# Kernel optimization log

Measured on AMD Instinct MI355X. Metric: run time of the kernel, lower is better.

## Reference

```python
import jax, jax.numpy as jnp
import numpy as np

B, T, H, D = 4, 2048, 16, 64
HID = H * D
ROPE_THETA = 10000.0


def _rope_tables(t, d, theta):
    # frequencies over half the head dim, duplicated to full head_dim
    inv_freq = 1.0 / (theta ** (np.arange(0, d, 2, dtype=np.float32) / d))  # (d/2,)
    pos = np.arange(t, dtype=np.float32)
    freqs = np.outer(pos, inv_freq)                      # (T, d/2)
    emb = np.concatenate([freqs, freqs], axis=-1)        # (T, d)
    return jnp.asarray(np.cos(emb)), jnp.asarray(np.sin(emb))


def setup_inputs() -> dict:
    key = jax.random.key(0)
    ks = jax.random.split(key, 5)
    s = 1.0 / np.sqrt(HID)
    cos, sin = _rope_tables(T, D, ROPE_THETA)
    return {
        "x": jax.random.normal(ks[0], (B, T, HID), dtype=jnp.float32),
        "cos": cos,
        "sin": sin,
        "wq": jax.random.normal(ks[1], (HID, HID), dtype=jnp.float32) * s,
        "wk": jax.random.normal(ks[2], (HID, HID), dtype=jnp.float32) * s,
        "wv": jax.random.normal(ks[3], (HID, HID), dtype=jnp.float32) * s,
        "wo": jax.random.normal(ks[4], (HID, HID), dtype=jnp.float32) * s,
    }


def _rotate_half(x):
    x1, x2 = jnp.split(x, 2, axis=-1)
    return jnp.concatenate([-x2, x1], axis=-1)


def reference(x, cos, sin, wq, wk, wv, wo):
    b, t, _ = x.shape
    # QKV projections (nn.Linear: y = x @ W^T), reshape to (B, H, T, D)
    q = (x @ wq.T).reshape(b, t, H, D).transpose(0, 2, 1, 3)
    k = (x @ wk.T).reshape(b, t, H, D).transpose(0, 2, 1, 3)
    v = (x @ wv.T).reshape(b, t, H, D).transpose(0, 2, 1, 3)
    # RoPE
    c = cos[None, None, :, :]
    s = sin[None, None, :, :]
    q = q * c + _rotate_half(q) * s
    k = k * c + _rotate_half(k) * s
    # causal SDPA
    scale = 1.0 / jnp.sqrt(jnp.asarray(D, dtype=x.dtype))
    scores = jnp.einsum("bhqd,bhkd->bhqk", q, k) * scale
    causal = jnp.tril(jnp.ones((t, t), dtype=bool))
    scores = jnp.where(causal[None, None], scores, jnp.finfo(scores.dtype).min)
    attn = jax.nn.softmax(scores, axis=-1)
    out = jnp.einsum("bhqk,bhkd->bhqd", attn, v)
    out = out.transpose(0, 2, 1, 3).reshape(b, t, HID)
    return out @ wo.T
```

## Files before the change

kernel.cpp:

```cpp
#include <hip/hip_runtime.h>

#define BSZ 4
#define TT 2048
#define NH 16
#define HD 64
#define HID 1024
#define BT 8192
#define BH 64

typedef unsigned short u16;
typedef unsigned int u32;
typedef unsigned long long u64;
typedef __attribute__((ext_vector_type(4))) float f32x4;
typedef __attribute__((ext_vector_type(8))) short bf16x8;

#define MFMA32(a, b, c) __builtin_amdgcn_mfma_f32_16x16x32_bf16(a, b, c, 0, 0, 0)

typedef const __attribute__((address_space(1))) u32* gp32;
typedef __attribute__((address_space(3))) u32* lp32;

__device__ __forceinline__ u16 f2bf(float f) {
    union { float f; u32 u; } x; x.f = f;
    u32 r = x.u + 0x7FFFu + ((x.u >> 16) & 1u);
    return (u16)(r >> 16);
}

__global__ __launch_bounds__(256) void cast_kernel(const float* __restrict__ src,
                                                   u16* __restrict__ dst, int n4) {
    int i = blockIdx.x * 256 + threadIdx.x;
    if (i >= n4) return;
    f32x4 v = *(const f32x4*)(src + (size_t)i * 4);
    uint2 u;
    u.x = (u32)f2bf(v[0]) | ((u32)f2bf(v[1]) << 16);
    u.y = (u32)f2bf(v[2]) | ((u32)f2bf(v[3]) << 16);
    *(uint2*)(dst + (size_t)i * 4) = u;
}

template<int MODE>
__global__ __launch_bounds__(256)
void gemm_bt(const u16* __restrict__ A, const u16* __restrict__ W,
             float* __restrict__ Cf, u16* __restrict__ qkv, u16* __restrict__ vt,
             const float* __restrict__ cosT, const float* __restrict__ sinT) {
    __shared__ u16 sh[128 * 128];
    u16* As = sh;
    u16* Bs = sh + 128 * 64;
    const int tid  = threadIdx.x;
    const int wv   = tid >> 6, lane = tid & 63;
    const int lrow = lane & 15, lk = lane >> 4;
    const int wm   = (wv & 1) * 64, wn = (wv >> 1) * 64;
    const int m0   = blockIdx.x * 128, n0 = blockIdx.y * 128;

    f32x4 acc[4][4] = {};

    for (int kk = 0; kk < HID; kk += 64) {
        __syncthreads();
        #pragma unroll
        for (int i = 0; i < 4; ++i) {
            int l16 = i * 256 + tid;
            int r = l16 >> 3, c = l16 & 7;
            int gc = (c ^ (r & 7)) * 8;
            __builtin_amdgcn_global_load_lds(
                (gp32)&A[(size_t)(m0 + r) * HID + kk + gc],
                (lp32)&As[l16 * 8], 16, 0, 0);
            __builtin_amdgcn_global_load_lds(
                (gp32)&W[(size_t)(n0 + r) * HID + kk + gc],
                (lp32)&Bs[l16 * 8], 16, 0, 0);
        }
        __syncthreads();

        #pragma unroll
        for (int k0 = 0; k0 < 64; k0 += 32) {
            bf16x8 af[4], bfr[4];
            #pragma unroll
            for (int i = 0; i < 4; ++i) {
                int row = wm + i * 16 + lrow;
                int pc  = ((k0 >> 3) + lk) ^ (row & 7);
                af[i] = *(const bf16x8*)&As[row * 64 + pc * 8];
            }
            #pragma unroll
            for (int j = 0; j < 4; ++j) {
                int row = wn + j * 16 + lrow;
                int pc  = ((k0 >> 3) + lk) ^ (row & 7);
                bfr[j] = *(const bf16x8*)&Bs[row * 64 + pc * 8];
            }
            #pragma unroll
            for (int i = 0; i < 4; ++i)
                #pragma unroll
                for (int j = 0; j < 4; ++j)
                    acc[i][j] = MFMA32(af[i], bfr[j], acc[i][j]);
        }
    }
    __syncthreads();

    if (MODE == 0) {
        if (blockIdx.y < 16) {
            const float QSC = (blockIdx.y < 8) ? 0.125f * 1.44269504f : 1.0f;
            #pragma unroll
            for (int i = 0; i < 4; ++i)
                #pragma unroll
                for (int r = 0; r < 4; ++r) {
                    int tl = (m0 + wm + i * 16 + lk * 4 + r) & (TT - 1);
                    #pragma unroll
                    for (int j = 0; j < 2; ++j) {
                        int dd = j * 16 + lrow;
                        float c = cosT[tl * HD + dd], s = sinT[tl * HD + dd];
                        float v1 = acc[i][j][r], v2 = acc[i][j + 2][r];
                        acc[i][j][r]     = (v1 * c - v2 * s) * QSC;
                        acc[i][j + 2][r] = (v2 * c + v1 * s) * QSC;
                    }
                }
        }
        #pragma unroll
        for (int i = 0; i < 4; ++i)
            #pragma unroll
            for (int j = 0; j < 4; ++j)
                #pragma unroll
                for (int r = 0; r < 4; ++r)
                    sh[(wm + i * 16 + lk * 4 + r) * 128 + wn + j * 16 + lrow] = f2bf(acc[i][j][r]);
        __syncthreads();
        const int b = m0 >> 11, tl0 = m0 & (TT - 1);
        if (blockIdx.y < 16) {
            #pragma unroll
            for (int p = 0; p < 8; ++p) {
                int idx = p * 256 + tid;
                int r = idx >> 4, c16 = idx & 15;
                f32x4 v = *(const f32x4*)&sh[r * 128 + c16 * 8];
                int nfull = n0 + c16 * 8;
                int proj = nfull >> 10, nl = nfull & 1023;
                int h = nl >> 6, d = nl & 63;
                u16* dst = qkv + (size_t)proj * BT * HID +
                           (((size_t)(b * NH + h) * TT + tl0 + r) * HD + d);
                *(f32x4*)dst = v;
            }
        } else {
            #pragma unroll
            for (int p = 0; p < 8; ++p) {
                int oc  = p * 256 + tid;
                int col = oc & 127;
                int t8  = oc >> 7;
                union { f32x4 v4; u16 u[8]; } u;
                #pragma unroll
                for (int j = 0; j < 8; ++j) u.u[j] = sh[(t8 * 8 + j) * 128 + col];
                int nl = ((n0 - 2048) + col);
                int h = nl >> 6, d = nl & 63;
                *(f32x4*)&vt[((size_t)(b * NH + h) * HD + d) * TT + tl0 + t8 * 8] = u.v4;
            }
        }
    } else {
        #pragma unroll
        for (int i = 0; i < 4; ++i)
            #pragma unroll
            for (int j = 0; j < 4; ++j)
                #pragma unroll
                for (int r = 0; r < 4; ++r) {
                    int m = m0 + wm + i * 16 + lk * 4 + r;
                    int n = n0 + wn + j * 16 + lrow;
                    Cf[(size_t)m * HID + n] = acc[i][j][r];
                }
    }
}

__device__ __forceinline__ u32 pkhu(float a, float b) {
    union { float f; u32 u; } xa, xb; xa.f = a; xb.f = b;
    return ((xa.u + 0x8000u) >> 16) | ((xb.u + 0x8000u) & 0xFFFF0000u);
}
__device__ __forceinline__ bf16x8 packP(const f32x4& a, const f32x4& b) {
    union { bf16x8 v; u32 w[4]; } u;
    u.w[0] = pkhu(a[0], a[1]); u.w[1] = pkhu(a[2], a[3]);
    u.w[2] = pkhu(b[0], b[1]); u.w[3] = pkhu(b[2], b[3]);
    return u.v;
}

__global__ __launch_bounds__(256)
void attn_kernel(const u16* __restrict__ q, const u16* __restrict__ k,
                 const u16* __restrict__ vt, u16* __restrict__ o) {
    __shared__ u16 Ks[64 * 72];
    __shared__ u16 Vts[64 * 72];
    const int tid  = threadIdx.x;
    const int w    = tid >> 6, lane = tid & 63;
    const int lrow = lane & 15, lk = lane >> 4;
    const int bh   = blockIdx.y;
    const int p    = blockIdx.x;
    const int q0a  = 64 * p, q0b = 64 * (31 - p);
    const size_t hb = (size_t)bh * TT * HD;

    bf16x8 qfa[2], qfb[2];
    #pragma unroll
    for (int kq = 0; kq < 2; ++kq) {
        qfa[kq] = *(const bf16x8*)&q[hb + (size_t)(q0a + w * 16 + lrow) * HD + kq * 32 + lk * 8];
        qfb[kq] = *(const bf16x8*)&q[hb + (size_t)(q0b + w * 16 + lrow) * HD + kq * 32 + lk * 8];
    }

    f32x4 oa[4] = {}, obc[4] = {};
    float lia = 0.f, lib = 0.f;

    const int r0 = tid >> 3, f0 = (tid & 7) * 8;
    const int r1 = (tid + 256) >> 3, f1 = (tid & 7) * 8;

    f32x4 pk0 = *(const f32x4*)&k[hb + (size_t)r0 * HD + f0];
    f32x4 pk1 = *(const f32x4*)&k[hb + (size_t)r1 * HD + f1];
    f32x4 pv0 = *(const f32x4*)&vt[hb + (size_t)r0 * TT + f0];
    f32x4 pv1 = *(const f32x4*)&vt[hb + (size_t)r1 * TT + f1];

    const int nIter = 32 - p;
    for (int it = 0; it < nIter; ++it) {
        const bool a_act = (it <= p);
        __syncthreads();
        *(f32x4*)&Ks[r0 * 72 + f0]  = pk0;
        *(f32x4*)&Ks[r1 * 72 + f1]  = pk1;
        *(f32x4*)&Vts[r0 * 72 + f0] = pv0;
        *(f32x4*)&Vts[r1 * 72 + f1] = pv1;
        __syncthreads();
        if (it + 1 < nIter) {
            const int nn = (it + 1) * 64;
            pk0 = *(const f32x4*)&k[hb + (size_t)(nn + r0) * HD + f0];
            pk1 = *(const f32x4*)&k[hb + (size_t)(nn + r1) * HD + f1];
            pv0 = *(const f32x4*)&vt[hb + (size_t)r0 * TT + nn + f0];
            pv1 = *(const f32x4*)&vt[hb + (size_t)r1 * TT + nn + f1];
        }

        bf16x8 kf0[4], kf1[4];
        #pragma unroll
        for (int mt = 0; mt < 4; ++mt) {
            kf0[mt] = *(const bf16x8*)&Ks[(mt * 16 + lrow) * 72 + lk * 8];
            kf1[mt] = *(const bf16x8*)&Ks[(mt * 16 + lrow) * 72 + 32 + lk * 8];
        }

        {
            f32x4 s[4] = {};
            #pragma unroll
            for (int mt = 0; mt < 4; ++mt) {
                s[mt] = MFMA32(kf0[mt], qfb[0], s[mt]);
                s[mt] = MFMA32(kf1[mt], qfb[1], s[mt]);
            }
            if (it == nIter - 1) {
                #pragma unroll
                for (int mt = 0; mt < 4; ++mt)
                    #pragma unroll
                    for (int r = 0; r < 4; ++r)
                        if (mt * 16 + lk * 4 + r > w * 16 + lrow) s[mt][r] = -1e30f;
            }
            #pragma unroll
            for (int mt = 0; mt < 4; ++mt)
                #pragma unroll
                for (int r = 0; r < 4; ++r) {
                    float pv = exp2f(s[mt][r]);
                    s[mt][r] = pv; lib += pv;
                }
            bf16x8 p0 = packP(s[0], s[1]), p1 = packP(s[2], s[3]);
            #pragma unroll
            for (int t2 = 0; t2 < 2; ++t2)
                #pragma unroll
                for (int dm = 0; dm < 4; ++dm) {
                    union { bf16x8 v; struct { u64 lo, hi; } u; } vf;
                    const u16* vrow = &Vts[(dm * 16 + lrow) * 72 + t2 * 32 + lk * 4];
                    vf.u.lo = *(const u64*)vrow;
                    vf.u.hi = *(const u64*)(vrow + 16);
                    obc[dm] = MFMA32(vf.v, t2 ? p1 : p0, obc[dm]);
                }
        }

        if (a_act) {
            f32x4 s[4] = {};
            #pragma unroll
            for (int mt = 0; mt < 4; ++mt) {
                s[mt] = MFMA32(kf0[mt], qfa[0], s[mt]);
                s[mt] = MFMA32(kf1[mt], qfa[1], s[mt]);
            }
            if (it == p) {
                #pragma unroll
                for (int mt = 0; mt < 4; ++mt)
                    #pragma unroll
                    for (int r = 0; r < 4; ++r)
                        if (mt * 16 + lk * 4 + r > w * 16 + lrow) s[mt][r] = -1e30f;
            }
            #pragma unroll
            for (int mt = 0; mt < 4; ++mt)
                #pragma unroll
                for (int r = 0; r < 4; ++r) {
                    float pv = exp2f(s[mt][r]);
                    s[mt][r] = pv; lia += pv;
                }
            bf16x8 p0 = packP(s[0], s[1]), p1 = packP(s[2], s[3]);
            #pragma unroll
            for (int t2 = 0; t2 < 2; ++t2)
                #pragma unroll
                for (int dm = 0; dm < 4; ++dm) {
                    union { bf16x8 v; struct { u64 lo, hi; } u; } vf;
                    const u16* vrow = &Vts[(dm * 16 + lrow) * 72 + t2 * 32 + lk * 4];
                    vf.u.lo = *(const u64*)vrow;
                    vf.u.hi = *(const u64*)(vrow + 16);
                    oa[dm] = MFMA32(vf.v, t2 ? p1 : p0, oa[dm]);
                }
        }
    }

    lia += __shfl_xor(lia, 16, 64); lia += __shfl_xor(lia, 32, 64);
    lib += __shfl_xor(lib, 16, 64); lib += __shfl_xor(lib, 32, 64);
    const int b = bh >> 4, h = bh & 15;
    const float inva = 1.f / lia, invb = 1.f / lib;
    #pragma unroll
    for (int dm = 0; dm < 4; ++dm) {
        uint2 pk;
        pk.x = (u32)f2bf(oa[dm][0] * inva) | ((u32)f2bf(oa[dm][1] * inva) << 16);
        pk.y = (u32)f2bf(oa[dm][2] * inva) | ((u32)f2bf(oa[dm][3] * inva) << 16);
        int row = q0a + w * 16 + lrow;
        *(uint2*)&o[((size_t)(b * TT + row)) * HID + h * HD + dm * 16 + lk * 4] = pk;
        pk.x = (u32)f2bf(obc[dm][0] * invb) | ((u32)f2bf(obc[dm][1] * invb) << 16);
        pk.y = (u32)f2bf(obc[dm][2] * invb) | ((u32)f2bf(obc[dm][3] * invb) << 16);
        row = q0b + w * 16 + lrow;
        *(uint2*)&o[((size_t)(b * TT + row)) * HID + h * HD + dm * 16 + lk * 4] = pk;
    }
}

extern "C" void kernel_launch(void* const* d_in, const int* in_sizes, int n_in,
                              void* d_out, int out_size, void* d_ws, size_t ws_size,
                              hipStream_t stream) {
    const float* x    = (const float*)d_in[0];
    const float* cosT = (const float*)d_in[1];
    const float* sinT = (const float*)d_in[2];
    const float* wq   = (const float*)d_in[3];
    const float* wk   = (const float*)d_in[4];
    const float* wv   = (const float*)d_in[5];
    const float* wo   = (const float*)d_in[6];
    float* out = (float*)d_out;

    char* ws = (char*)d_ws;
    size_t off = 0;
    u16* x_bf  = (u16*)(ws + off); off += (size_t)BT * HID * 2;
    u16* wqkv  = (u16*)(ws + off); off += (size_t)3 * HID * HID * 2;
    u16* wo_bf = (u16*)(ws + off); off += (size_t)HID * HID * 2;
    u16* qb    = (u16*)(ws + off); off += (size_t)BT * HID * 2;
    u16* kb    = (u16*)(ws + off); off += (size_t)BT * HID * 2;
    u16* vtb   = (u16*)(ws + off); off += (size_t)BT * HID * 2;
    u16* ob    = (u16*)(ws + off); off += (size_t)BT * HID * 2;
    (void)kb;

    cast_kernel<<<(BT * HID / 4 + 255) / 256, 256, 0, stream>>>(x, x_bf, BT * HID / 4);
    cast_kernel<<<1024, 256, 0, stream>>>(wq, wqkv, HID * HID / 4);
    cast_kernel<<<1024, 256, 0, stream>>>(wk, wqkv + (size_t)HID * HID, HID * HID / 4);
    cast_kernel<<<1024, 256, 0, stream>>>(wv, wqkv + (size_t)2 * HID * HID, HID * HID / 4);
    cast_kernel<<<1024, 256, 0, stream>>>(wo, wo_bf, HID * HID / 4);

    gemm_bt<0><<<dim3(BT / 128, 3 * HID / 128), 256, 0, stream>>>(
        x_bf, wqkv, nullptr, qb, vtb, cosT, sinT);

    attn_kernel<<<dim3(16, BH), 256, 0, stream>>>(qb, kb, vtb, ob);

    gemm_bt<1><<<dim3(BT / 128, HID / 128), 256, 0, stream>>>(
        ob, wo_bf, out, nullptr, nullptr, nullptr, nullptr);
}
```

Before: 286.8 us.

## Load K/V fragments directly from global in attention; merge weight casts

The attention kernel drops its LDS staging of K and V^T tiles and the two block barriers per iteration. Each wave now loads its MFMA fragments straight from global memory, relying on L1/L2 for reuse across the four waves. The four weight-cast launches are merged into one kernel to cut launch overhead. The trade-off is more global/L1 traffic, since each wave reloads the same tiles. It also loses the software prefetch into registers, so load latency is exposed unless the compiler overlaps it.

```diff
diff --git a/kernel.cpp b/kernel.cpp
--- a/kernel.cpp
+++ b/kernel.cpp
@@ -29,6 +29,21 @@
                                                    u16* __restrict__ dst, int n4) {
     int i = blockIdx.x * 256 + threadIdx.x;
     if (i >= n4) return;
+    f32x4 v = *(const f32x4*)(src + (size_t)i * 4);
+    uint2 u;
+    u.x = (u32)f2bf(v[0]) | ((u32)f2bf(v[1]) << 16);
+    u.y = (u32)f2bf(v[2]) | ((u32)f2bf(v[3]) << 16);
+    *(uint2*)(dst + (size_t)i * 4) = u;
+}
+
+__global__ __launch_bounds__(256) void cast4_kernel(const float* __restrict__ w0,
+        const float* __restrict__ w1, const float* __restrict__ w2,
+        const float* __restrict__ w3, u16* __restrict__ d0, u16* __restrict__ d1,
+        u16* __restrict__ d2, u16* __restrict__ d3) {
+    int blk = blockIdx.x, seg = blk >> 10;
+    const float* src = (seg == 0) ? w0 : (seg == 1) ? w1 : (seg == 2) ? w2 : w3;
+    u16* dst = (seg == 0) ? d0 : (seg == 1) ? d1 : (seg == 2) ? d2 : d3;
+    int i = (blk & 1023) * 256 + threadIdx.x;
     f32x4 v = *(const f32x4*)(src + (size_t)i * 4);
     uint2 u;
     u.x = (u32)f2bf(v[0]) | ((u32)f2bf(v[1]) << 16);
@@ -174,8 +189,6 @@
 __global__ __launch_bounds__(256)
 void attn_kernel(const u16* __restrict__ q, const u16* __restrict__ k,
                  const u16* __restrict__ vt, u16* __restrict__ o) {
-    __shared__ u16 Ks[64 * 72];
-    __shared__ u16 Vts[64 * 72];
     const int tid  = threadIdx.x;
     const int w    = tid >> 6, lane = tid & 63;
     const int lrow = lane & 15, lk = lane >> 4;
@@ -194,36 +207,29 @@
     f32x4 oa[4] = {}, obc[4] = {};
     float lia = 0.f, lib = 0.f;
 
-    const int r0 = tid >> 3, f0 = (tid & 7) * 8;
-    const int r1 = (tid + 256) >> 3, f1 = (tid & 7) * 8;
-
-    f32x4 pk0 = *(const f32x4*)&k[hb + (size_t)r0 * HD + f0];
-    f32x4 pk1 = *(const f32x4*)&k[hb + (size_t)r1 * HD + f1];
-    f32x4 pv0 = *(const f32x4*)&vt[hb + (size_t)r0 * TT + f0];
-    f32x4 pv1 = *(const f32x4*)&vt[hb + (size_t)r1 * TT + f1];
+    const u16* krow = &k[hb + (size_t)lrow * HD + lk * 8];
+    const u16* vrow = &vt[hb + (size_t)lrow * TT + lk * 4];
 
     const int nIter = 32 - p;
     for (int it = 0; it < nIter; ++it) {
+        const int n0 = it * 64;
         const bool a_act = (it <= p);
-        __syncthreads();
-        *(f32x4*)&Ks[r0 * 72 + f0]  = pk0;
-        *(f32x4*)&Ks[r1 * 72 + f1]  = pk1;
-        *(f32x4*)&Vts[r0 * 72 + f0] = pv0;
-        *(f32x4*)&Vts[r1 * 72 + f1] = pv1;
-        __syncthreads();
-        if (it + 1 < nIter) {
-            const int nn = (it + 1) * 64;
-            pk0 = *(const f32x4*)&k[hb + (size_t)(nn + r0) * HD + f0];
-            pk1 = *(const f32x4*)&k[hb + (size_t)(nn + r1) * HD + f1];
-            pv0 = *(const f32x4*)&vt[hb + (size_t)r0 * TT + nn + f0];
-            pv1 = *(const f32x4*)&vt[hb + (size_t)r1 * TT + nn + f1];
-        }
 
         bf16x8 kf0[4], kf1[4];
         #pragma unroll
         for (int mt = 0; mt < 4; ++mt) {
-            kf0[mt] = *(const bf16x8*)&Ks[(mt * 16 + lrow) * 72 + lk * 8];
-            kf1[mt] = *(const bf16x8*)&Ks[(mt * 16 + lrow) * 72 + 32 + lk * 8];
+            const u16* kr = krow + (size_t)(n0 + mt * 16) * HD;
+            kf0[mt] = *(const bf16x8*)kr;
+            kf1[mt] = *(const bf16x8*)(kr + 32);
+        }
+        u64 vlo[2][4], vhi[2][4];
+        #pragma unroll
+        for (int dm = 0; dm < 4; ++dm) {
+            const u16* vr = vrow + (size_t)(dm * 16) * TT + n0;
+            vlo[0][dm] = *(const u64*)vr;
+            vhi[0][dm] = *(const u64*)(vr + 16);
+            vlo[1][dm] = *(const u64*)(vr + 32);
+            vhi[1][dm] = *(const u64*)(vr + 48);
         }
 
         {
@@ -253,9 +259,7 @@
                 #pragma unroll
                 for (int dm = 0; dm < 4; ++dm) {
                     union { bf16x8 v; struct { u64 lo, hi; } u; } vf;
-                    const u16* vrow = &Vts[(dm * 16 + lrow) * 72 + t2 * 32 + lk * 4];
-                    vf.u.lo = *(const u64*)vrow;
-                    vf.u.hi = *(const u64*)(vrow + 16);
+                    vf.u.lo = vlo[t2][dm]; vf.u.hi = vhi[t2][dm];
                     obc[dm] = MFMA32(vf.v, t2 ? p1 : p0, obc[dm]);
                 }
         }
@@ -287,9 +291,7 @@
                 #pragma unroll
                 for (int dm = 0; dm < 4; ++dm) {
                     union { bf16x8 v; struct { u64 lo, hi; } u; } vf;
-                    const u16* vrow = &Vts[(dm * 16 + lrow) * 72 + t2 * 32 + lk * 4];
-                    vf.u.lo = *(const u64*)vrow;
-                    vf.u.hi = *(const u64*)(vrow + 16);
+                    vf.u.lo = vlo[t2][dm]; vf.u.hi = vhi[t2][dm];
                     oa[dm] = MFMA32(vf.v, t2 ? p1 : p0, oa[dm]);
                 }
         }
@@ -334,13 +336,10 @@
     u16* kb    = (u16*)(ws + off); off += (size_t)BT * HID * 2;
     u16* vtb   = (u16*)(ws + off); off += (size_t)BT * HID * 2;
     u16* ob    = (u16*)(ws + off); off += (size_t)BT * HID * 2;
-    (void)kb;
 
     cast_kernel<<<(BT * HID / 4 + 255) / 256, 256, 0, stream>>>(x, x_bf, BT * HID / 4);
-    cast_kernel<<<1024, 256, 0, stream>>>(wq, wqkv, HID * HID / 4);
-    cast_kernel<<<1024, 256, 0, stream>>>(wk, wqkv + (size_t)HID * HID, HID * HID / 4);
-    cast_kernel<<<1024, 256, 0, stream>>>(wv, wqkv + (size_t)2 * HID * HID, HID * HID / 4);
-    cast_kernel<<<1024, 256, 0, stream>>>(wo, wo_bf, HID * HID / 4);
+    cast4_kernel<<<4096, 256, 0, stream>>>(wq, wk, wv, wo,
+        wqkv, wqkv + (size_t)HID * HID, wqkv + (size_t)2 * HID * HID, wo_bf);
 
     gemm_bt<0><<<dim3(BT / 128, 3 * HID / 128), 256, 0, stream>>>(
         x_bf, wqkv, nullptr, qb, vtb, cosT, sinT);
```

Result: slower. 528.8 us (+84.4%).

## Split paired causal attention blocks into one-tile blocks and fuse weight casts

Applied to the files above, without the earlier changes.

The attention kernel previously had each block process two query tiles (p and 31-p) to balance causal work. Now each block handles a single 64-row query tile, the grid doubles to 32x64, and heavier tiles are scheduled first by reversing blockIdx. This gives more blocks and lower register pressure per block, at the cost of loading each K/V tile in two blocks instead of sharing it. The four weight cast launches are also merged into one kernel, which removes launch overhead.

```diff
diff --git a/kernel.cpp b/kernel.cpp
--- a/kernel.cpp
+++ b/kernel.cpp
@@ -29,6 +29,21 @@
                                                    u16* __restrict__ dst, int n4) {
     int i = blockIdx.x * 256 + threadIdx.x;
     if (i >= n4) return;
+    f32x4 v = *(const f32x4*)(src + (size_t)i * 4);
+    uint2 u;
+    u.x = (u32)f2bf(v[0]) | ((u32)f2bf(v[1]) << 16);
+    u.y = (u32)f2bf(v[2]) | ((u32)f2bf(v[3]) << 16);
+    *(uint2*)(dst + (size_t)i * 4) = u;
+}
+
+__global__ __launch_bounds__(256) void cast4_kernel(const float* __restrict__ w0,
+        const float* __restrict__ w1, const float* __restrict__ w2,
+        const float* __restrict__ w3, u16* __restrict__ d0, u16* __restrict__ d1,
+        u16* __restrict__ d2, u16* __restrict__ d3) {
+    int blk = blockIdx.x, seg = blk >> 10;
+    const float* src = (seg == 0) ? w0 : (seg == 1) ? w1 : (seg == 2) ? w2 : w3;
+    u16* dst = (seg == 0) ? d0 : (seg == 1) ? d1 : (seg == 2) ? d2 : d3;
+    int i = (blk & 1023) * 256 + threadIdx.x;
     f32x4 v = *(const f32x4*)(src + (size_t)i * 4);
     uint2 u;
     u.x = (u32)f2bf(v[0]) | ((u32)f2bf(v[1]) << 16);
@@ -180,31 +195,28 @@
     const int w    = tid >> 6, lane = tid & 63;
     const int lrow = lane & 15, lk = lane >> 4;
     const int bh   = blockIdx.y;
-    const int p    = blockIdx.x;
-    const int q0a  = 64 * p, q0b = 64 * (31 - p);
+    const int s_i  = 31 - blockIdx.x;
+    const int q0   = 64 * s_i;
     const size_t hb = (size_t)bh * TT * HD;
 
-    bf16x8 qfa[2], qfb[2];
+    bf16x8 qf[2];
     #pragma unroll
-    for (int kq = 0; kq < 2; ++kq) {
-        qfa[kq] = *(const bf16x8*)&q[hb + (size_t)(q0a + w * 16 + lrow) * HD + kq * 32 + lk * 8];
-        qfb[kq] = *(const bf16x8*)&q[hb + (size_t)(q0b + w * 16 + lrow) * HD + kq * 32 + lk * 8];
-    }
-
-    f32x4 oa[4] = {}, obc[4] = {};
-    float lia = 0.f, lib = 0.f;
+    for (int kq = 0; kq < 2; ++kq)
+        qf[kq] = *(const bf16x8*)&q[hb + (size_t)(q0 + w * 16 + lrow) * HD + kq * 32 + lk * 8];
+
+    f32x4 oacc[4] = {};
+    float li = 0.f;
 
     const int r0 = tid >> 3, f0 = (tid & 7) * 8;
-    const int r1 = (tid + 256) >> 3, f1 = (tid & 7) * 8;
+    const int r1 = r0 + 32, f1 = f0;
 
     f32x4 pk0 = *(const f32x4*)&k[hb + (size_t)r0 * HD + f0];
     f32x4 pk1 = *(const f32x4*)&k[hb + (size_t)r1 * HD + f1];
     f32x4 pv0 = *(const f32x4*)&vt[hb + (size_t)r0 * TT + f0];
     f32x4 pv1 = *(const f32x4*)&vt[hb + (size_t)r1 * TT + f1];
 
-    const int nIter = 32 - p;
+    const int nIter = s_i + 1;
     for (int it = 0; it < nIter; ++it) {
-        const bool a_act = (it <= p);
         __syncthreads();
         *(f32x4*)&Ks[r0 * 72 + f0]  = pk0;
         *(f32x4*)&Ks[r1 * 72 + f1]  = pk1;
@@ -219,96 +231,50 @@
             pv1 = *(const f32x4*)&vt[hb + (size_t)r1 * TT + nn + f1];
         }
 
-        bf16x8 kf0[4], kf1[4];
+        f32x4 s[4] = {};
         #pragma unroll
         for (int mt = 0; mt < 4; ++mt) {
-            kf0[mt] = *(const bf16x8*)&Ks[(mt * 16 + lrow) * 72 + lk * 8];
-            kf1[mt] = *(const bf16x8*)&Ks[(mt * 16 + lrow) * 72 + 32 + lk * 8];
-        }
-
-        {
-            f32x4 s[4] = {};
-            #pragma unroll
-            for (int mt = 0; mt < 4; ++mt) {
-                s[mt] = MFMA32(kf0[mt], qfb[0], s[mt]);
-                s[mt] = MFMA32(kf1[mt], qfb[1], s[mt]);
-            }
-            if (it == nIter - 1) {
-                #pragma unroll
-                for (int mt = 0; mt < 4; ++mt)
-                    #pragma unroll
-                    for (int r = 0; r < 4; ++r)
-                        if (mt * 16 + lk * 4 + r > w * 16 + lrow) s[mt][r] = -1e30f;
-            }
+            bf16x8 kf0 = *(const bf16x8*)&Ks[(mt * 16 + lrow) * 72 + lk * 8];
+            bf16x8 kf1 = *(const bf16x8*)&Ks[(mt * 16 + lrow) * 72 + 32 + lk * 8];
+            s[mt] = MFMA32(kf0, qf[0], s[mt]);
+            s[mt] = MFMA32(kf1, qf[1], s[mt]);
+        }
+        if (it == nIter - 1) {
             #pragma unroll
             for (int mt = 0; mt < 4; ++mt)
                 #pragma unroll
-                for (int r = 0; r < 4; ++r) {
-                    float pv = exp2f(s[mt][r]);
-                    s[mt][r] = pv; lib += pv;
-                }
-            bf16x8 p0 = packP(s[0], s[1]), p1 = packP(s[2], s[3]);
-            #pragma unroll
-            for (int t2 = 0; t2 < 2; ++t2)
-                #pragma unroll
-                for (int dm = 0; dm < 4; ++dm) {
-                    union { bf16x8 v; struct { u64 lo, hi; } u; } vf;
-                    const u16* vrow = &Vts[(dm * 16 + lrow) * 72 + t2 * 32 + lk * 4];
-                    vf.u.lo = *(const u64*)vrow;
-                    vf.u.hi = *(const u64*)(vrow + 16);
-                    obc[dm] = MFMA32(vf.v, t2 ? p1 : p0, obc[dm]);
-                }
-        }
-
-        if (a_act) {
-            f32x4 s[4] = {};
-            #pragma unroll
-            for (int mt = 0; mt < 4; ++mt) {
-                s[mt] = MFMA32(kf0[mt], qfa[0], s[mt]);
-                s[mt] = MFMA32(kf1[mt], qfa[1], s[mt]);
-            }
-            if (it == p) {
-                #pragma unroll
-                for (int mt = 0; mt < 4; ++mt)
-                    #pragma unroll
-                    for (int r = 0; r < 4; ++r)
-                        if (mt * 16 + lk * 4 + r > w * 16 + lrow) s[mt][r] = -1e30f;
-            }
-            #pragma unroll
-            for (int mt = 0; mt < 4; ++mt)
-                #pragma unroll
-                for (int r = 0; r < 4; ++r) {
-                    float pv = exp2f(s[mt][r]);
-                    s[mt][r] = pv; lia += pv;
-                }
-            bf16x8 p0 = packP(s[0], s[1]), p1 = packP(s[2], s[3]);
-            #pragma unroll
-            for (int t2 = 0; t2 < 2; ++t2)
-                #pragma unroll
-                for (int dm = 0; dm < 4; ++dm) {
-                    union { bf16x8 v; struct { u64 lo, hi; } u; } vf;
-                    const u16* vrow = &Vts[(dm * 16 + lrow) * 72 + t2 * 32 + lk * 4];
-                    vf.u.lo = *(const u64*)vrow;
-                    vf.u.hi = *(const u64*)(vrow + 16);
-                    oa[dm] = MFMA32(vf.v, t2 ? p1 : p0, oa[dm]);
-                }
-        }
+                for (int r = 0; r < 4; ++r)
+                    if (mt * 16 + lk * 4 + r > w * 16 + lrow) s[mt][r] = -1e30f;
+        }
+        #pragma unroll
+        for (int mt = 0; mt < 4; ++mt)
+            #pragma unroll
+            for (int r = 0; r < 4; ++r) {
+                float pv = exp2f(s[mt][r]);
+                s[mt][r] = pv; li += pv;
+            }
+        bf16x8 p0 = packP(s[0], s[1]), p1 = packP(s[2], s[3]);
+        #pragma unroll
+        for (int t2 = 0; t2 < 2; ++t2)
+            #pragma unroll
+            for (int dm = 0; dm < 4; ++dm) {
+                union { bf16x8 v; struct { u64 lo, hi; } u; } vf;
+                const u16* vrow = &Vts[(dm * 16 + lrow) * 72 + t2 * 32 + lk * 4];
+                vf.u.lo = *(const u64*)vrow;
+                vf.u.hi = *(const u64*)(vrow + 16);
+                oacc[dm] = MFMA32(vf.v, t2 ? p1 : p0, oacc[dm]);
+            }
     }
 
-    lia += __shfl_xor(lia, 16, 64); lia += __shfl_xor(lia, 32, 64);
-    lib += __shfl_xor(lib, 16, 64); lib += __shfl_xor(lib, 32, 64);
+    li += __shfl_xor(li, 16, 64); li += __shfl_xor(li, 32, 64);
     const int b = bh >> 4, h = bh & 15;
-    const float inva = 1.f / lia, invb = 1.f / lib;
+    const float inv = 1.f / li;
+    const int row = q0 + w * 16 + lrow;
     #pragma unroll
     for (int dm = 0; dm < 4; ++dm) {
         uint2 pk;
-        pk.x = (u32)f2bf(oa[dm][0] * inva) | ((u32)f2bf(oa[dm][1] * inva) << 16);
-        pk.y = (u32)f2bf(oa[dm][2] * inva) | ((u32)f2bf(oa[dm][3] * inva) << 16);
-        int row = q0a + w * 16 + lrow;
-        *(uint2*)&o[((size_t)(b * TT + row)) * HID + h * HD + dm * 16 + lk * 4] = pk;
-        pk.x = (u32)f2bf(obc[dm][0] * invb) | ((u32)f2bf(obc[dm][1] * invb) << 16);
-        pk.y = (u32)f2bf(obc[dm][2] * invb) | ((u32)f2bf(obc[dm][3] * invb) << 16);
-        row = q0b + w * 16 + lrow;
+        pk.x = (u32)f2bf(oacc[dm][0] * inv) | ((u32)f2bf(oacc[dm][1] * inv) << 16);
+        pk.y = (u32)f2bf(oacc[dm][2] * inv) | ((u32)f2bf(oacc[dm][3] * inv) << 16);
         *(uint2*)&o[((size_t)(b * TT + row)) * HID + h * HD + dm * 16 + lk * 4] = pk;
     }
 }
@@ -334,18 +300,15 @@
     u16* kb    = (u16*)(ws + off); off += (size_t)BT * HID * 2;
     u16* vtb   = (u16*)(ws + off); off += (size_t)BT * HID * 2;
     u16* ob    = (u16*)(ws + off); off += (size_t)BT * HID * 2;
-    (void)kb;
 
     cast_kernel<<<(BT * HID / 4 + 255) / 256, 256, 0, stream>>>(x, x_bf, BT * HID / 4);
-    cast_kernel<<<1024, 256, 0, stream>>>(wq, wqkv, HID * HID / 4);
-    cast_kernel<<<1024, 256, 0, stream>>>(wk, wqkv + (size_t)HID * HID, HID * HID / 4);
-    cast_kernel<<<1024, 256, 0, stream>>>(wv, wqkv + (size_t)2 * HID * HID, HID * HID / 4);
-    cast_kernel<<<1024, 256, 0, stream>>>(wo, wo_bf, HID * HID / 4);
+    cast4_kernel<<<4096, 256, 0, stream>>>(wq, wk, wv, wo,
+        wqkv, wqkv + (size_t)HID * HID, wqkv + (size_t)2 * HID * HID, wo_bf);
 
     gemm_bt<0><<<dim3(BT / 128, 3 * HID / 128), 256, 0, stream>>>(
         x_bf, wqkv, nullptr, qb, vtb, cosT, sinT);
 
-    attn_kernel<<<dim3(16, BH), 256, 0, stream>>>(qb, kb, vtb, ob);
+    attn_kernel<<<dim3(32, BH), 256, 0, stream>>>(qb, kb, vtb, ob);
 
     gemm_bt<1><<<dim3(BT / 128, HID / 128), 256, 0, stream>>>(
         ob, wo_bf, out, nullptr, nullptr, nullptr, nullptr);
```

After: 316.7 us. +10.4%, slower.
